# Performance work log

Hardware: AMD Instinct MI355X
Metric: run time of the kernel (lower is better)

Reference implementation:

```python
import jax, jax.numpy as jnp
import numpy as np

B, T, D_IN, D_H = 256, 256, 128, 512


def setup_inputs() -> dict:
    key = jax.random.key(0)
    ks = jax.random.split(key, 12)
    s = 1.0 / np.sqrt(D_H)
    u = lambda k, shape: jax.random.uniform(k, shape, jnp.float32, -s, s)
    X = jax.random.normal(ks[0], (B, T, D_IN), jnp.float32)
    missing_mask = (jax.random.uniform(ks[1], (B, T, D_IN)) < 0.8).astype(jnp.float32)
    return dict(
        X=X, missing_mask=missing_mask,
        W_ih0=u(ks[2], (3 * D_H, D_IN)), W_hh0=u(ks[3], (3 * D_H, D_H)),
        b_ih0=u(ks[4], (3 * D_H,)), b_hh0=u(ks[5], (3 * D_H,)),
        W_ih1=u(ks[6], (3 * D_H, D_H)), W_hh1=u(ks[7], (3 * D_H, D_H)),
        b_ih1=u(ks[8], (3 * D_H,)), b_hh1=u(ks[9], (3 * D_H,)),
        W_out=u(ks[10], (D_IN, D_H)), b_out=u(ks[11], (D_IN,)),
    )


def _gru_cell(x, h, W_ih, W_hh, b_ih, b_hh):
    # torch.nn.GRUCell math; gate order r, z, n
    gi = x @ W_ih.T + b_ih          # [B, 3H]
    gh = h @ W_hh.T + b_hh          # [B, 3H]
    ir, iz, in_ = jnp.split(gi, 3, axis=-1)
    hr, hz, hn = jnp.split(gh, 3, axis=-1)
    r = jax.nn.sigmoid(ir + hr)
    z = jax.nn.sigmoid(iz + hz)
    n = jnp.tanh(in_ + r * hn)
    return (1.0 - z) * n + z * h


def reference(X, missing_mask, W_ih0, W_hh0, b_ih0, b_hh0,
              W_ih1, W_hh1, b_ih1, b_hh1, W_out, b_out):
    bz = X.shape[0]
    h0 = jnp.zeros((bz, D_H), X.dtype)

    def step(h, xm):
        x, m = xm                                   # [B, D_IN] each
        est = h @ W_out.T + b_out                   # estimation from previous hidden
        imputed = m * x + (1.0 - m) * est           # per-step imputation masking
        h = _gru_cell(imputed, h, W_ih0, W_hh0, b_ih0, b_hh0)
        h = _gru_cell(h, h, W_ih1, W_hh1, b_ih1, b_hh1)  # layer>0: input == hidden (as in source)
        return h, (est, imputed, h)

    xs = (jnp.swapaxes(X, 0, 1), jnp.swapaxes(missing_mask, 0, 1))  # time-major
    h_final, (pre, out, hs) = jax.lax.scan(step, h0, xs)
    pre_collector = jnp.swapaxes(pre, 0, 1)          # [B, T, D_IN]
    output_collector = jnp.swapaxes(out, 0, 1)       # [B, T, D_IN]
    hidden_state_collector = jnp.swapaxes(hs, 0, 1)  # [B, T, D_H]
    final_est = (h_final @ W_out.T + b_out)[:, None, :]
    output_collector = jnp.concatenate([output_collector[:, 1:], final_est], axis=1)
    return (pre_collector, output_collector, h_final, hidden_state_collector)
```

## Files before the change

### kernel.cpp

```cpp
#include <hip/hip_runtime.h>
#include <cstdint>
#include <cstddef>


#define BB  256
#define TT  256
#define DIN 128
#define DH  512

typedef __attribute__((ext_vector_type(8))) short short8;
typedef __attribute__((ext_vector_type(4))) float f32x4;
typedef __attribute__((ext_vector_type(4))) unsigned int u32x4;
typedef unsigned short u16;
typedef unsigned long long u64;

#define OFF_BAR   0
#define OFF_HBF   256
#define OFF_H1BF  (OFF_HBF + BB*DH/2)
#define OFF_WOUT  (OFF_H1BF + BB*DH/2)
#define OFF_WHH0  (OFF_WOUT + (DIN*DH)/2)
#define OFF_WIH0  (OFF_WHH0 + (3*DH*DH)/2)
#define OFF_WIH1  (OFF_WIH0 + (3*DH*DIN)/2)
#define OFF_WHH1  (OFF_WIH1 + (3*DH*DH)/2)
#define WS_FLOATS (OFF_WHH1 + (3*DH*DH)/2)

__device__ __forceinline__ float sigm(float x)   { return 1.0f / (1.0f + __expf(-x)); }
__device__ __forceinline__ float tanh_f(float x) { return 2.0f / (1.0f + __expf(-2.0f * x)) - 1.0f; }

__device__ __forceinline__ u16 f2bf(float x) {
    unsigned u = __builtin_bit_cast(unsigned, x);
    u += 0x7fffu + ((u >> 16) & 1u);
    return (u16)(u >> 16);
}

__device__ __forceinline__ u32x4 ld_b128_sc(const void* p) {
    u32x4 r;
    asm volatile("global_load_dwordx4 %0, %1, off sc0 sc1" : "=v"(r) : "v"(p));
    return r;
}
__device__ __forceinline__ void st_b128_sc(void* p, u32x4 v) {
    asm volatile("global_store_dwordx4 %0, %1, off sc0 sc1" :: "v"(p), "v"(v) : "memory");
}

__device__ __forceinline__ void group_bar(unsigned* bar, unsigned target) {
    asm volatile("s_waitcnt vmcnt(0)" ::: "memory");
    __syncthreads();
    if (threadIdx.x == 0) {
        __hip_atomic_fetch_add(bar, 1u, __ATOMIC_RELAXED, __HIP_MEMORY_SCOPE_AGENT);
        while (__hip_atomic_load(bar, __ATOMIC_RELAXED, __HIP_MEMORY_SCOPE_AGENT) < target) {
            __builtin_amdgcn_s_sleep(1);
        }
    }
    __syncthreads();
}

__global__ void prep_kernel(const float* __restrict__ Wout, const float* __restrict__ Whh0,
                            const float* __restrict__ Wih0, const float* __restrict__ Wih1,
                            const float* __restrict__ Whh1, float* __restrict__ ws) {
    u16* dOut = (u16*)(ws + OFF_WOUT);
    u16* dHH0 = (u16*)(ws + OFF_WHH0);
    u16* dIH0 = (u16*)(ws + OFF_WIH0);
    u16* dIH1 = (u16*)(ws + OFF_WIH1);
    u16* dHH1 = (u16*)(ws + OFF_WHH1);
    const int N0 = DIN * DH, N1 = 3 * DH * DH, N2 = 3 * DH * DIN;
    const int total = N0 + 3 * N1 + N2;
    for (int i = blockIdx.x * 256 + threadIdx.x; i < total; i += gridDim.x * 256) {
        int j = i;
        if (j < N0) { dOut[j] = f2bf(Wout[j]); continue; } j -= N0;
        if (j < N1) { dHH0[j] = f2bf(Whh0[j]); continue; } j -= N1;
        if (j < N2) { dIH0[j] = f2bf(Wih0[j]); continue; } j -= N2;
        if (j < N1) { dIH1[j] = f2bf(Wih1[j]); continue; } j -= N1;
        dHH1[j] = f2bf(Whh1[j]);
    }
}

__global__ __launch_bounds__(512) void rnn_kernel(
    const float* __restrict__ X,    const float* __restrict__ Mm,
    const float* __restrict__ bih0, const float* __restrict__ bhh0,
    const float* __restrict__ bih1, const float* __restrict__ bhh1,
    const float* __restrict__ bout,
    float* __restrict__ out, float* __restrict__ ws)
{
    __shared__ __align__(16) u16 Atile[16 * 520];
    __shared__ __align__(16) u16 IMPL[16 * 136];
    __shared__ __align__(16) u16 Sbf[16][2][16];
    __shared__ float ghL[3][2][16][17];
    __shared__ float cplane[2][3][256];
    __shared__ __align__(16) float H32L[16][36];
    __shared__ __align__(16) float H132L[16][36];

    u16*   Hbf  = (u16*)(ws + OFF_HBF);
    u16*   H1bf = (u16*)(ws + OFF_H1BF);
    const u16* WbOut = (const u16*)(ws + OFF_WOUT);
    const u16* WbHH0 = (const u16*)(ws + OFF_WHH0);
    const u16* WbIH0 = (const u16*)(ws + OFF_WIH0);
    const u16* WbIH1 = (const u16*)(ws + OFF_WIH1);
    const u16* WbHH1 = (const u16*)(ws + OFF_WHH1);

    float* pre  = out;
    float* outc = out + BB * TT * DIN;
    float* hfin = out + 2 * BB * TT * DIN;
    float* hsc  = hfin + BB * DH;

    const int tid  = threadIdx.x;
    const int lane = tid & 63;
    const int v    = tid >> 6;
    const int fg   = blockIdx.x & 15;
    const int bb   = blockIdx.x >> 4;
    const int m_   = lane & 15;
    const int q    = lane >> 4;
    const int q8   = q * 8;
    const int rowB = bb * 16 + q * 4;
    const int lrow = q * 4;

    unsigned* bar = (unsigned*)(ws + OFF_BAR) + bb * 16;
    unsigned ep = 0;

    for (int i = tid; i < 16 * 36; i += 512) ((float*)H32L)[i] = 0.f;

    const int fE  = v * 16 + m_;
    const int g   = v >> 1, ft = v & 1;
    const int fp  = g * DH + (fg + 16 * ft) * 16 + m_;
    const u16* BwE = WbOut + (size_t)fE * DH;
    const u16* BwG = WbHH0 + (size_t)fp * DH;
    const float bo  = bout[fE];
    const float bhG = (v < 6) ? bhh0[fp] : 0.f;

    const int ffA = (fg + 16 * v) * 16 + m_;
    const u16* B0 = WbIH0 + (size_t)ffA * DIN;
    const u16* B1 = B0 + (size_t)DH * DIN;
    const u16* B2 = B1 + (size_t)DH * DIN;
    const float bi0 = (v < 2) ? bih0[ffA] : 0.f;
    const float bi1 = (v < 2) ? bih0[DH + ffA] : 0.f;
    const float bi2 = (v < 2) ? bih0[2 * DH + ffA] : 0.f;

    const int ft3 = (v < 3) ? 0 : 1;
    const int g3  = v - 3 * ft3;
    const int ffB0 = (fg + 16 * ft3) * 16;
    const int gf  = g3 * DH + ffB0 + m_;
    const u16* Bi = WbIH1 + (size_t)gf * DH;
    const u16* Bh = WbHH1 + (size_t)gf * DH;
    const float biB = (v < 6) ? bih1[gf] : 0.f;
    const float bhB = (v < 6) ? bhh1[gf] : 0.f;

    const int sr_ = tid >> 6, sc_ = tid & 63;

    for (int t = 0; t <= TT; ++t) {
        float xv[4], mv[4];
        if (t < TT) {
            #pragma unroll
            for (int r = 0; r < 4; ++r) {
                const int xi = ((rowB + r) * TT + t) * DIN + fE;
                xv[r] = X[xi]; mv[r] = Mm[xi];
            }
        }
        {
            const u16* src = Hbf + bb * 16 * DH;
            u32x4 d0 = ld_b128_sc(src + sr_ * DH + sc_ * 8);
            u32x4 d1 = ld_b128_sc(src + (sr_ + 8) * DH + sc_ * 8);
            asm volatile("s_waitcnt vmcnt(0)" ::: "memory");
            *(u32x4*)(Atile + sr_ * 520 + sc_ * 8) = d0;
            *(u32x4*)(Atile + (sr_ + 8) * 520 + sc_ * 8) = d1;
        }
        __syncthreads();

        f32x4 aE = {0.f, 0.f, 0.f, 0.f}, aG = aE;
        if (v < 6) {
            #pragma unroll 4
            for (int kb = 0; kb < DH; kb += 32) {
                short8 a = *(const short8*)(Atile + m_ * 520 + kb + q8);
                aE = __builtin_amdgcn_mfma_f32_16x16x32_bf16(a, *(const short8*)(BwE + kb + q8), aE, 0, 0, 0);
                aG = __builtin_amdgcn_mfma_f32_16x16x32_bf16(a, *(const short8*)(BwG + kb + q8), aG, 0, 0, 0);
            }
        } else {
            #pragma unroll 4
            for (int kb = 0; kb < DH; kb += 32) {
                short8 a = *(const short8*)(Atile + m_ * 520 + kb + q8);
                aE = __builtin_amdgcn_mfma_f32_16x16x32_bf16(a, *(const short8*)(BwE + kb + q8), aE, 0, 0, 0);
            }
        }

        if (t == TT) {
            if (v == fg) {
                #pragma unroll
                for (int r = 0; r < 4; ++r)
                    outc[((rowB + r) * TT + TT - 1) * DIN + fE] = aE[r] + bo;
            }
            break;
        }
        #pragma unroll
        for (int r = 0; r < 4; ++r) {
            const float est = aE[r] + bo;
            const float imp = mv[r] * xv[r] + (1.f - mv[r]) * est;
            IMPL[(lrow + r) * 136 + fE] = f2bf(imp);
            if (v == fg) {
                const int xi = ((rowB + r) * TT + t) * DIN + fE;
                pre[xi] = est;
                if (t > 0) outc[xi - DIN] = imp;
            }
        }
        if (v < 6) {
            #pragma unroll
            for (int r = 0; r < 4; ++r) ghL[g][ft][lrow + r][m_] = aG[r] + bhG;
        }
        __syncthreads();

        if (v < 2) {
            f32x4 a0 = {0.f,0.f,0.f,0.f}, a1 = a0, a2 = a0;
            #pragma unroll
            for (int kb = 0; kb < DIN; kb += 32) {
                short8 a = *(const short8*)(IMPL + m_ * 136 + kb + q8);
                a0 = __builtin_amdgcn_mfma_f32_16x16x32_bf16(a, *(const short8*)(B0 + kb + q8), a0, 0, 0, 0);
                a1 = __builtin_amdgcn_mfma_f32_16x16x32_bf16(a, *(const short8*)(B1 + kb + q8), a1, 0, 0, 0);
                a2 = __builtin_amdgcn_mfma_f32_16x16x32_bf16(a, *(const short8*)(B2 + kb + q8), a2, 0, 0, 0);
            }
            const int lc = v * 16 + m_;
            #pragma unroll
            for (int r = 0; r < 4; ++r) {
                const float rr = sigm(a0[r] + bi0 + ghL[0][v][lrow + r][m_]);
                const float zz = sigm(a1[r] + bi1 + ghL[1][v][lrow + r][m_]);
                const float nn = tanh_f(a2[r] + bi2 + rr * ghL[2][v][lrow + r][m_]);
                const float hp = H32L[lrow + r][lc];
                const float h1 = (1.f - zz) * nn + zz * hp;
                H132L[lrow + r][lc] = h1;
                Sbf[lrow + r][v][m_] = f2bf(h1);
            }
        }
        __syncthreads();
        if (tid < 64) {
            const int row = tid >> 2, sl = (tid >> 1) & 1, hf = tid & 1;
            const int col = (fg + 16 * sl) * 16 + hf * 8;
            st_b128_sc(H1bf + (bb * 16 + row) * DH + col, *(const u32x4*)&Sbf[row][sl][hf * 8]);
        }
        group_bar(bar, (++ep) * 16);

        {
            const u16* src = H1bf + bb * 16 * DH;
            u32x4 d0 = ld_b128_sc(src + sr_ * DH + sc_ * 8);
            u32x4 d1 = ld_b128_sc(src + (sr_ + 8) * DH + sc_ * 8);
            asm volatile("s_waitcnt vmcnt(0)" ::: "memory");
            *(u32x4*)(Atile + sr_ * 520 + sc_ * 8) = d0;
            *(u32x4*)(Atile + (sr_ + 8) * 520 + sc_ * 8) = d1;
        }
        __syncthreads();

        float sr4[4];
        if (v < 6) {
            f32x4 ai = {0.f,0.f,0.f,0.f}, ah = ai;
            #pragma unroll 4
            for (int kb = 0; kb < DH; kb += 32) {
                short8 a = *(const short8*)(Atile + m_ * 520 + kb + q8);
                ai = __builtin_amdgcn_mfma_f32_16x16x32_bf16(a, *(const short8*)(Bi + kb + q8), ai, 0, 0, 0);
                ah = __builtin_amdgcn_mfma_f32_16x16x32_bf16(a, *(const short8*)(Bh + kb + q8), ah, 0, 0, 0);
            }
            if (g3 == 0) {
                #pragma unroll
                for (int r = 0; r < 4; ++r) sr4[r] = ai[r] + ah[r] + biB + bhB;
            } else if (g3 == 1) {
                #pragma unroll
                for (int r = 0; r < 4; ++r) cplane[ft3][0][m_ * 16 + q * 4 + r] = ai[r] + ah[r] + biB + bhB;
            } else {
                #pragma unroll
                for (int r = 0; r < 4; ++r) {
                    cplane[ft3][1][m_ * 16 + q * 4 + r] = ai[r] + biB;
                    cplane[ft3][2][m_ * 16 + q * 4 + r] = ah[r] + bhB;
                }
            }
        }
        __syncthreads();
        if (v == 0 || v == 3) {
            const int lc = ft3 * 16 + m_;
            #pragma unroll
            for (int r = 0; r < 4; ++r) {
                const int idx = m_ * 16 + q * 4 + r;
                const float rr = sigm(sr4[r]);
                const float zz = sigm(cplane[ft3][0][idx]);
                const float nn = tanh_f(cplane[ft3][1][idx] + rr * cplane[ft3][2][idx]);
                const float h1 = H132L[lrow + r][lc];
                const float hn = (1.f - zz) * nn + zz * h1;
                H32L[lrow + r][lc] = hn;
                Sbf[lrow + r][ft3][m_] = f2bf(hn);
            }
        }
        __syncthreads();
        if (tid < 64) {
            const int row = tid >> 2, sl = (tid >> 1) & 1, hf = tid & 1;
            const int col = (fg + 16 * sl) * 16 + hf * 8;
            st_b128_sc(Hbf + (bb * 16 + row) * DH + col, *(const u32x4*)&Sbf[row][sl][hf * 8]);
        }
        if (tid < 128) {
            const int row = tid >> 3, sl = (tid >> 2) & 1, c4 = tid & 3;
            const int col = (fg + 16 * sl) * 16 + c4 * 4;
            const int b = bb * 16 + row;
            u32x4 val = *(const u32x4*)&H32L[row][sl * 16 + c4 * 4];
            *(u32x4*)(hsc + ((size_t)b * TT + t) * DH + col) = val;
            if (t == TT - 1) *(u32x4*)(hfin + (size_t)b * DH + col) = val;
        }
        group_bar(bar, (++ep) * 16);
    }
}

extern "C" void kernel_launch(void* const* d_in, const int* in_sizes, int n_in,
                              void* d_out, int out_size, void* d_ws, size_t ws_size,
                              hipStream_t stream) {
    const float* X    = (const float*)d_in[0];
    const float* Mm   = (const float*)d_in[1];
    const float* Wih0 = (const float*)d_in[2];
    const float* Whh0 = (const float*)d_in[3];
    const float* bih0 = (const float*)d_in[4];
    const float* bhh0 = (const float*)d_in[5];
    const float* Wih1 = (const float*)d_in[6];
    const float* Whh1 = (const float*)d_in[7];
    const float* bih1 = (const float*)d_in[8];
    const float* bhh1 = (const float*)d_in[9];
    const float* Wout = (const float*)d_in[10];
    const float* bout = (const float*)d_in[11];
    float* out = (float*)d_out;
    float* ws  = (float*)d_ws;

    hipMemsetAsync(d_ws, 0, (size_t)(OFF_H1BF) * sizeof(float), stream);

    hipLaunchKernelGGL(prep_kernel, dim3(1024), dim3(256), 0, stream,
                       Wout, Whh0, Wih0, Wih1, Whh1, ws);

    hipLaunchKernelGGL(rnn_kernel, dim3(256), dim3(512), 0, stream,
                       X, Mm, bih0, bhh0, bih1, bhh1, bout, out, ws);
}
```

Measured before the change: 5.250 ms.

## Replace group barriers with per-producer flags and a gather warp for streaming K-chunks

Each group-wide atomic barrier is replaced by per-block flags that producers set after storing their hidden-state slice. A dedicated warp (v==7) polls those flags and copies the ready 32-column chunks into double LDS buffers, publishing per-chunk sequence numbers. Compute warps spin on each chunk, so MFMA accumulation starts as soon as partial data arrives instead of waiting for the whole group. Work that warp 7 used to do is folded into warp 6, and weight loads are software-prefetched one step ahead. The cost is heavier spinning and polling traffic, and correctness now depends on flag ordering and memory visibility.

```diff
diff --git a/kernel.cpp b/kernel.cpp
--- a/kernel.cpp
+++ b/kernel.cpp
@@ -14,8 +14,8 @@
 typedef unsigned short u16;
 typedef unsigned long long u64;
 
-#define OFF_BAR   0
-#define OFF_HBF   256
+#define OFF_FLAGS 0
+#define OFF_HBF   8192
 #define OFF_H1BF  (OFF_HBF + BB*DH/2)
 #define OFF_WOUT  (OFF_H1BF + BB*DH/2)
 #define OFF_WHH0  (OFF_WOUT + (DIN*DH)/2)
@@ -41,17 +41,68 @@
 __device__ __forceinline__ void st_b128_sc(void* p, u32x4 v) {
     asm volatile("global_store_dwordx4 %0, %1, off sc0 sc1" :: "v"(p), "v"(v) : "memory");
 }
-
-__device__ __forceinline__ void group_bar(unsigned* bar, unsigned target) {
-    asm volatile("s_waitcnt vmcnt(0)" ::: "memory");
-    __syncthreads();
-    if (threadIdx.x == 0) {
-        __hip_atomic_fetch_add(bar, 1u, __ATOMIC_RELAXED, __HIP_MEMORY_SCOPE_AGENT);
-        while (__hip_atomic_load(bar, __ATOMIC_RELAXED, __HIP_MEMORY_SCOPE_AGENT) < target) {
-            __builtin_amdgcn_s_sleep(1);
-        }
+__device__ __forceinline__ unsigned ld_flag(const unsigned* p) {
+    unsigned r;
+    asm volatile("global_load_dword %0, %1, off sc0 sc1\n\ts_waitcnt vmcnt(0)"
+                 : "=v"(r) : "v"(p) : "memory");
+    return r;
+}
+__device__ __forceinline__ void st_flag(unsigned* p, unsigned v) {
+    asm volatile("global_store_dword %0, %1, off sc0 sc1" :: "v"(p), "v"(v) : "memory");
+}
+
+__device__ __forceinline__ void spin_seq(unsigned* s, unsigned tag) {
+    while (__hip_atomic_load(s, __ATOMIC_RELAXED, __HIP_MEMORY_SCOPE_WORKGROUP) < tag)
+        __builtin_amdgcn_s_sleep(1);
+    asm volatile("" ::: "memory");
+}
+
+__device__ __forceinline__ void gather16(const u16* src, u16* lbuf,
+                                         const unsigned* F, unsigned gtag,
+                                         unsigned* seq, unsigned stag, int lane) {
+    const int p16 = lane & 15;
+    const int row = lane >> 2, co = (lane & 3) * 8;
+    const unsigned* myflag = F + p16 * 16;
+    unsigned done = 0;
+    while (done != 0xFFu) {
+        unsigned f = ld_flag(myflag);
+        unsigned prod = (unsigned)__ballot(f >= gtag) & 0xFFFFu;
+        unsigned prm  = prod & (prod >> 1) & 0x5555u;
+        unsigned want = 0;
+        #pragma unroll
+        for (int j = 0; j < 8; ++j) want |= ((prm >> (2 * j)) & 1u) << j;
+        want &= ~done;
+        if (want) {
+            u32x4 d0[8], d1[8];
+            #pragma unroll
+            for (int j = 0; j < 8; ++j) {
+                if (want & (1u << j)) {
+                    d0[j] = ld_b128_sc(src + (size_t)row * DH + j * 32 + co);
+                    d1[j] = ld_b128_sc(src + (size_t)row * DH + 256 + j * 32 + co);
+                }
+            }
+            asm volatile("s_waitcnt vmcnt(0)" ::: "memory");
+            #pragma unroll
+            for (int j = 0; j < 8; ++j) {
+                if (want & (1u << j)) {
+                    *(u32x4*)(lbuf + row * 520 + j * 32 + co) = d0[j];
+                    *(u32x4*)(lbuf + row * 520 + 256 + j * 32 + co) = d1[j];
+                }
+            }
+            asm volatile("s_waitcnt lgkmcnt(0)" ::: "memory");
+            if (lane == 0) {
+                #pragma unroll
+                for (int j = 0; j < 8; ++j) {
+                    if (want & (1u << j)) {
+                        __hip_atomic_store(&seq[j], stag, __ATOMIC_RELAXED, __HIP_MEMORY_SCOPE_WORKGROUP);
+                        __hip_atomic_store(&seq[j + 8], stag, __ATOMIC_RELAXED, __HIP_MEMORY_SCOPE_WORKGROUP);
+                    }
+                }
+            }
+            done |= want;
+        }
+        if (done != 0xFFu) __builtin_amdgcn_s_sleep(1);
     }
-    __syncthreads();
 }
 
 __global__ void prep_kernel(const float* __restrict__ Wout, const float* __restrict__ Whh0,
@@ -74,6 +125,8 @@
     }
 }
 
+#define MFMA(A,B,C) __builtin_amdgcn_mfma_f32_16x16x32_bf16((A),(B),(C),0,0,0)
+
 __global__ __launch_bounds__(512) void rnn_kernel(
     const float* __restrict__ X,    const float* __restrict__ Mm,
     const float* __restrict__ bih0, const float* __restrict__ bhh0,
@@ -81,13 +134,15 @@
     const float* __restrict__ bout,
     float* __restrict__ out, float* __restrict__ ws)
 {
-    __shared__ __align__(16) u16 Atile[16 * 520];
+    __shared__ __align__(16) u16 bufA[16 * 520];
+    __shared__ __align__(16) u16 bufB[16 * 520];
     __shared__ __align__(16) u16 IMPL[16 * 136];
     __shared__ __align__(16) u16 Sbf[16][2][16];
     __shared__ float ghL[3][2][16][17];
     __shared__ float cplane[2][3][256];
     __shared__ __align__(16) float H32L[16][36];
     __shared__ __align__(16) float H132L[16][36];
+    __shared__ unsigned seqA[16], seqB[16];
 
     u16*   Hbf  = (u16*)(ws + OFF_HBF);
     u16*   H1bf = (u16*)(ws + OFF_H1BF);
@@ -113,17 +168,25 @@
     const int rowB = bb * 16 + q * 4;
     const int lrow = q * 4;
 
-    unsigned* bar = (unsigned*)(ws + OFF_BAR) + bb * 16;
-    unsigned ep = 0;
+    unsigned* FLG = (unsigned*)(ws + OFF_FLAGS);
+    unsigned* F0  = FLG + ((0 * 16 + bb) * 16) * 16;
+    unsigned* F1  = FLG + ((1 * 16 + bb) * 16) * 16;
+    unsigned* myF0 = F0 + fg * 16;
+    unsigned* myF1 = F1 + fg * 16;
 
     for (int i = tid; i < 16 * 36; i += 512) ((float*)H32L)[i] = 0.f;
-
-    const int fE  = v * 16 + m_;
-    const int g   = v >> 1, ft = v & 1;
-    const int fp  = g * DH + (fg + 16 * ft) * 16 + m_;
-    const u16* BwE = WbOut + (size_t)fE * DH;
-    const u16* BwG = WbHH0 + (size_t)fp * DH;
-    const float bo  = bout[fE];
+    if (tid < 16) { seqA[tid] = 0u; seqB[tid] = 0u; }
+    __syncthreads();
+
+    const int fE   = v * 16 + m_;
+    const int fE2  = 112 + m_;
+    const int g    = v >> 1, ft = v & 1;
+    const int fp   = g * DH + (fg + 16 * ft) * 16 + m_;
+    const u16* BwE  = WbOut + (size_t)fE * DH;
+    const u16* BwE2 = WbOut + (size_t)fE2 * DH;
+    const u16* BwG  = WbHH0 + (size_t)fp * DH;
+    const float bo  = (v < 7) ? bout[fE] : 0.f;
+    const float bo2 = bout[fE2];
     const float bhG = (v < 6) ? bhh0[fp] : 0.f;
 
     const int ffA = (fg + 16 * v) * 16 + m_;
@@ -136,72 +199,100 @@
 
     const int ft3 = (v < 3) ? 0 : 1;
     const int g3  = v - 3 * ft3;
-    const int ffB0 = (fg + 16 * ft3) * 16;
-    const int gf  = g3 * DH + ffB0 + m_;
+    const int gf  = g3 * DH + (fg + 16 * ft3) * 16 + m_;
     const u16* Bi = WbIH1 + (size_t)gf * DH;
     const u16* Bh = WbHH1 + (size_t)gf * DH;
     const float biB = (v < 6) ? bih1[gf] : 0.f;
     const float bhB = (v < 6) ? bhh1[gf] : 0.f;
 
-    const int sr_ = tid >> 6, sc_ = tid & 63;
+    const u16* srcA = Hbf  + (size_t)bb * 16 * DH;
+    const u16* srcB = H1bf + (size_t)bb * 16 * DH;
 
     for (int t = 0; t <= TT; ++t) {
-        float xv[4], mv[4];
-        if (t < TT) {
+        const unsigned stag = (unsigned)(t + 1);
+        float xv[4], mv[4], xv2[4], mv2[4];
+        if (v < 7 && t < TT) {
             #pragma unroll
             for (int r = 0; r < 4; ++r) {
                 const int xi = ((rowB + r) * TT + t) * DIN + fE;
                 xv[r] = X[xi]; mv[r] = Mm[xi];
             }
-        }
-        {
-            const u16* src = Hbf + bb * 16 * DH;
-            u32x4 d0 = ld_b128_sc(src + sr_ * DH + sc_ * 8);
-            u32x4 d1 = ld_b128_sc(src + (sr_ + 8) * DH + sc_ * 8);
-            asm volatile("s_waitcnt vmcnt(0)" ::: "memory");
-            *(u32x4*)(Atile + sr_ * 520 + sc_ * 8) = d0;
-            *(u32x4*)(Atile + (sr_ + 8) * 520 + sc_ * 8) = d1;
-        }
-        __syncthreads();
-
-        f32x4 aE = {0.f, 0.f, 0.f, 0.f}, aG = aE;
-        if (v < 6) {
-            #pragma unroll 4
-            for (int kb = 0; kb < DH; kb += 32) {
-                short8 a = *(const short8*)(Atile + m_ * 520 + kb + q8);
-                aE = __builtin_amdgcn_mfma_f32_16x16x32_bf16(a, *(const short8*)(BwE + kb + q8), aE, 0, 0, 0);
-                aG = __builtin_amdgcn_mfma_f32_16x16x32_bf16(a, *(const short8*)(BwG + kb + q8), aG, 0, 0, 0);
-            }
+            if (v == 6) {
+                #pragma unroll
+                for (int r = 0; r < 4; ++r) {
+                    const int xi = ((rowB + r) * TT + t) * DIN + fE2;
+                    xv2[r] = X[xi]; mv2[r] = Mm[xi];
+                }
+            }
+        }
+
+        f32x4 aE = {0.f,0.f,0.f,0.f}, aE2 = aE, aG = aE;
+        if (v == 7) {
+            gather16(srcA, bufA, F1, (unsigned)t, seqA, stag, lane);
         } else {
-            #pragma unroll 4
-            for (int kb = 0; kb < DH; kb += 32) {
-                short8 a = *(const short8*)(Atile + m_ * 520 + kb + q8);
-                aE = __builtin_amdgcn_mfma_f32_16x16x32_bf16(a, *(const short8*)(BwE + kb + q8), aE, 0, 0, 0);
+            short8 wE = *(const short8*)(BwE + q8);
+            short8 wE2, wG;
+            if (v == 6) wE2 = *(const short8*)(BwE2 + q8);
+            if (v < 6)  wG  = *(const short8*)(BwG + q8);
+            for (int p = 0; p < 16; ++p) {
+                spin_seq(&seqA[p], stag);
+                short8 a = *(const short8*)(bufA + m_ * 520 + p * 32 + q8);
+                short8 nE = wE, nE2 = wE2, nG = wG;
+                if (p < 15) {
+                    nE = *(const short8*)(BwE + (p + 1) * 32 + q8);
+                    if (v == 6) nE2 = *(const short8*)(BwE2 + (p + 1) * 32 + q8);
+                    if (v < 6)  nG  = *(const short8*)(BwG + (p + 1) * 32 + q8);
+                }
+                aE = MFMA(a, wE, aE);
+                if (v == 6) aE2 = MFMA(a, wE2, aE2);
+                if (v < 6)  aG  = MFMA(a, wG, aG);
+                wE = nE; wE2 = nE2; wG = nG;
             }
         }
 
         if (t == TT) {
-            if (v == fg) {
+            if (v == fg && v < 7) {
                 #pragma unroll
                 for (int r = 0; r < 4; ++r)
                     outc[((rowB + r) * TT + TT - 1) * DIN + fE] = aE[r] + bo;
             }
+            if (v == 6 && fg == 7) {
+                #pragma unroll
+                for (int r = 0; r < 4; ++r)
+                    outc[((rowB + r) * TT + TT - 1) * DIN + fE2] = aE2[r] + bo2;
+            }
             break;
         }
-        #pragma unroll
-        for (int r = 0; r < 4; ++r) {
-            const float est = aE[r] + bo;
-            const float imp = mv[r] * xv[r] + (1.f - mv[r]) * est;
-            IMPL[(lrow + r) * 136 + fE] = f2bf(imp);
-            if (v == fg) {
-                const int xi = ((rowB + r) * TT + t) * DIN + fE;
-                pre[xi] = est;
-                if (t > 0) outc[xi - DIN] = imp;
-            }
-        }
-        if (v < 6) {
-            #pragma unroll
-            for (int r = 0; r < 4; ++r) ghL[g][ft][lrow + r][m_] = aG[r] + bhG;
+
+        if (v < 7) {
+            #pragma unroll
+            for (int r = 0; r < 4; ++r) {
+                const float est = aE[r] + bo;
+                const float imp = mv[r] * xv[r] + (1.f - mv[r]) * est;
+                IMPL[(lrow + r) * 136 + fE] = f2bf(imp);
+                if (v == fg) {
+                    const int xi = ((rowB + r) * TT + t) * DIN + fE;
+                    pre[xi] = est;
+                    if (t > 0) outc[xi - DIN] = imp;
+                }
+            }
+            if (v == 6) {
+                #pragma unroll
+                for (int r = 0; r < 4; ++r) {
+                    const float est = aE2[r] + bo2;
+                    const float imp = mv2[r] * xv2[r] + (1.f - mv2[r]) * est;
+                    IMPL[(lrow + r) * 136 + fE2] = f2bf(imp);
+                    if (fg == 7) {
+                        const int xi = ((rowB + r) * TT + t) * DIN + fE2;
+                        pre[xi] = est;
+                        if (t > 0) outc[xi - DIN] = imp;
+                    }
+                }
+            }
+            if (v < 6) {
+                #pragma unroll
+                for (int r = 0; r < 4; ++r) ghL[g][ft][lrow + r][m_] = aG[r] + bhG;
+            }
         }
         __syncthreads();
 
@@ -210,9 +301,9 @@
             #pragma unroll
             for (int kb = 0; kb < DIN; kb += 32) {
                 short8 a = *(const short8*)(IMPL + m_ * 136 + kb + q8);
-                a0 = __builtin_amdgcn_mfma_f32_16x16x32_bf16(a, *(const short8*)(B0 + kb + q8), a0, 0, 0, 0);
-                a1 = __builtin_amdgcn_mfma_f32_16x16x32_bf16(a, *(const short8*)(B1 + kb + q8), a1, 0, 0, 0);
-                a2 = __builtin_amdgcn_mfma_f32_16x16x32_bf16(a, *(const short8*)(B2 + kb + q8), a2, 0, 0, 0);
+                a0 = MFMA(a, *(const short8*)(B0 + kb + q8), a0);
+                a1 = MFMA(a, *(const short8*)(B1 + kb + q8), a1);
+                a2 = MFMA(a, *(const short8*)(B2 + kb + q8), a2);
             }
             const int lc = v * 16 + m_;
             #pragma unroll
@@ -230,35 +321,38 @@
         if (tid < 64) {
             const int row = tid >> 2, sl = (tid >> 1) & 1, hf = tid & 1;
             const int col = (fg + 16 * sl) * 16 + hf * 8;
-            st_b128_sc(H1bf + (bb * 16 + row) * DH + col, *(const u32x4*)&Sbf[row][sl][hf * 8]);
-        }
-        group_bar(bar, (++ep) * 16);
-
-        {
-            const u16* src = H1bf + bb * 16 * DH;
-            u32x4 d0 = ld_b128_sc(src + sr_ * DH + sc_ * 8);
-            u32x4 d1 = ld_b128_sc(src + (sr_ + 8) * DH + sc_ * 8);
+            st_b128_sc(H1bf + (size_t)(bb * 16 + row) * DH + col,
+                       *(const u32x4*)&Sbf[row][sl][hf * 8]);
             asm volatile("s_waitcnt vmcnt(0)" ::: "memory");
-            *(u32x4*)(Atile + sr_ * 520 + sc_ * 8) = d0;
-            *(u32x4*)(Atile + (sr_ + 8) * 520 + sc_ * 8) = d1;
-        }
-        __syncthreads();
+            if (tid == 0) st_flag(myF0, stag);
+        }
 
         float sr4[4];
-        if (v < 6) {
-            f32x4 ai = {0.f,0.f,0.f,0.f}, ah = ai;
-            #pragma unroll 4
-            for (int kb = 0; kb < DH; kb += 32) {
-                short8 a = *(const short8*)(Atile + m_ * 520 + kb + q8);
-                ai = __builtin_amdgcn_mfma_f32_16x16x32_bf16(a, *(const short8*)(Bi + kb + q8), ai, 0, 0, 0);
-                ah = __builtin_amdgcn_mfma_f32_16x16x32_bf16(a, *(const short8*)(Bh + kb + q8), ah, 0, 0, 0);
+        f32x4 ai = {0.f,0.f,0.f,0.f}, ah = ai;
+        if (v == 7) {
+            gather16(srcB, bufB, F0, stag, seqB, stag, lane);
+        } else if (v < 6) {
+            short8 wI = *(const short8*)(Bi + q8);
+            short8 wH = *(const short8*)(Bh + q8);
+            for (int p = 0; p < 16; ++p) {
+                spin_seq(&seqB[p], stag);
+                short8 a = *(const short8*)(bufB + m_ * 520 + p * 32 + q8);
+                short8 nI = wI, nH = wH;
+                if (p < 15) {
+                    nI = *(const short8*)(Bi + (p + 1) * 32 + q8);
+                    nH = *(const short8*)(Bh + (p + 1) * 32 + q8);
+                }
+                ai = MFMA(a, wI, ai);
+                ah = MFMA(a, wH, ah);
+                wI = nI; wH = nH;
             }
             if (g3 == 0) {
                 #pragma unroll
                 for (int r = 0; r < 4; ++r) sr4[r] = ai[r] + ah[r] + biB + bhB;
             } else if (g3 == 1) {
                 #pragma unroll
-                for (int r = 0; r < 4; ++r) cplane[ft3][0][m_ * 16 + q * 4 + r] = ai[r] + ah[r] + biB + bhB;
+                for (int r = 0; r < 4; ++r)
+                    cplane[ft3][0][m_ * 16 + q * 4 + r] = ai[r] + ah[r] + biB + bhB;
             } else {
                 #pragma unroll
                 for (int r = 0; r < 4; ++r) {
@@ -286,17 +380,19 @@
         if (tid < 64) {
             const int row = tid >> 2, sl = (tid >> 1) & 1, hf = tid & 1;
             const int col = (fg + 16 * sl) * 16 + hf * 8;
-            st_b128_sc(Hbf + (bb * 16 + row) * DH + col, *(const u32x4*)&Sbf[row][sl][hf * 8]);
-        }
-        if (tid < 128) {
-            const int row = tid >> 3, sl = (tid >> 2) & 1, c4 = tid & 3;
+            st_b128_sc(Hbf + (size_t)(bb * 16 + row) * DH + col,
+                       *(const u32x4*)&Sbf[row][sl][hf * 8]);
+            asm volatile("s_waitcnt vmcnt(0)" ::: "memory");
+            if (tid == 0) st_flag(myF1, stag);
+        } else if (tid >= 128 && tid < 256) {
+            const int k = tid - 128;
+            const int row = k >> 3, sl = (k >> 2) & 1, c4 = k & 3;
             const int col = (fg + 16 * sl) * 16 + c4 * 4;
             const int b = bb * 16 + row;
             u32x4 val = *(const u32x4*)&H32L[row][sl * 16 + c4 * 4];
             *(u32x4*)(hsc + ((size_t)b * TT + t) * DH + col) = val;
             if (t == TT - 1) *(u32x4*)(hfin + (size_t)b * DH + col) = val;
         }
-        group_bar(bar, (++ep) * 16);
     }
 }
 
```

Result: faster. 4.884 ms (-7.0%).
